# Optimization experiments

Hardware: AMD Instinct MI355X
Metric: run time of the kernel (lower is better)

The kernel has to match this reference:

```python
import jax, jax.numpy as jnp
import numpy as np

NHEADS = 8
LN_EPS = 1e-5

def _layer_norm(x, g, b):
    mu = jnp.mean(x, axis=-1, keepdims=True)
    var = jnp.mean((x - mu) ** 2, axis=-1, keepdims=True)
    return (x - mu) * jax.lax.rsqrt(var + LN_EPS) * g + b

def setup_inputs() -> dict:
    key = jax.random.key(0)
    ks = jax.random.split(key, 12)
    B, L, D = 8, 1024, 512
    F = 2 * D  # ffn_dim = 2*dim
    std = 0.01  # init_weights: Linear weights ~ N(0, 0.01), biases zero
    inp = {
        'query': jax.random.normal(ks[0], (B, L, D), dtype=jnp.float32),
        'q_mask': jnp.ones((B, L), dtype=jnp.int32),
        'wq': jax.random.normal(ks[1], (D, D), dtype=jnp.float32) * std,
        'bq': jnp.zeros((D,), dtype=jnp.float32),
        'wk': jax.random.normal(ks[2], (D, D), dtype=jnp.float32) * std,
        'bk': jnp.zeros((D,), dtype=jnp.float32),
        'wv': jax.random.normal(ks[3], (D, D), dtype=jnp.float32) * std,
        'bv': jnp.zeros((D,), dtype=jnp.float32),
        'wo': jax.random.normal(ks[4], (D, D), dtype=jnp.float32) * std,
        'bo': jnp.zeros((D,), dtype=jnp.float32),
        'ln1_g': jnp.ones((D,), dtype=jnp.float32),
        'ln1_b': jnp.zeros((D,), dtype=jnp.float32),
        'w1': jax.random.normal(ks[5], (D, F), dtype=jnp.float32) * std,
        'b1': jnp.zeros((F,), dtype=jnp.float32),
        'w2': jax.random.normal(ks[6], (F, D), dtype=jnp.float32) * std,
        'b2': jnp.zeros((D,), dtype=jnp.float32),
        'ln2_g': jnp.ones((D,), dtype=jnp.float32),
        'ln2_b': jnp.zeros((D,), dtype=jnp.float32),
    }
    return inp

def reference(query, q_mask, wq, bq, wk, bk, wv, bv, wo, bo, ln1_g, ln1_b, w1, b1, w2, b2, ln2_g, ln2_b):
    B, L, D = query.shape
    H = NHEADS
    dh = D // H
    residual = query
    # projections (dropout in eval mode -> identity)
    q = query @ wq + bq
    k = query @ wk + bk
    v = query @ wv + bv
    # faithful to torch .view(batch*nheads, -1, dim_head) (no head transpose)
    q = q.reshape(B * H, L, dh)
    k = k.reshape(B * H, L, dh)
    v = v.reshape(B * H, L, dh)
    # faithful to torch mask.repeat(nheads, 1) -> tile along batch dim
    mf = q_mask.astype(jnp.float32)
    qm = jnp.tile(mf, (H, 1))  # [B*H, L]
    km = qm
    mask = qm[:, :, None] * km[:, None, :]  # [B*H, L, L] outer product
    scores = jnp.einsum('bqd,bkd->bqk', q, k) / np.sqrt(dh).astype(np.float32)
    A = jnp.where(mask == 0, 0.0, jnp.exp(scores))  # masked_fill(-inf).exp()
    A_sum = jnp.maximum(jnp.sum(A, axis=-1, keepdims=True), 1.0)
    attn = A / A_sum
    context = jnp.einsum('bqk,bkd->bqd', attn, v).reshape(B, L, H * dh)
    out = context @ wo + bo
    out = _layer_norm(residual + out, ln1_g, ln1_b)
    # positional-wise FFN: Linear -> ReLU -> Linear, residual + LayerNorm
    ffn = jax.nn.relu(out @ w1 + b1) @ w2 + b2
    out2 = _layer_norm(out + ffn, ln2_g, ln2_b)
    return (out2, q_mask, query, query, q_mask)
```

## Files before the change

kernel.cpp:

```cpp
#include <hip/hip_runtime.h>
#include <hip/hip_bf16.h>

typedef __hip_bfloat16 bf16;
typedef __attribute__((ext_vector_type(4))) float f32x4;
typedef __attribute__((ext_vector_type(8))) short s16x8;

#define MFMA(a, b, c) __builtin_amdgcn_mfma_f32_16x16x32_bf16((a), (b), (c), 0, 0, 0)

__device__ __forceinline__ void g2l16(const bf16* g, bf16* l) {
  __builtin_amdgcn_global_load_lds((const __attribute__((address_space(1))) void*)g,
                                   (__attribute__((address_space(3))) void*)l,
                                   16, 0, 0);
}
__device__ __forceinline__ bf16 cvt_bf(float f) { return __float2bfloat16(f); }
__device__ __forceinline__ float bf2f(bf16 h) { return __bfloat162float(h); }

__global__ __launch_bounds__(256)
void wcvt_all_k(const float* __restrict__ wq, const float* __restrict__ wk,
                const float* __restrict__ wv, const float* __restrict__ wo,
                const float* __restrict__ w1, const float* __restrict__ w2,
                bf16* __restrict__ wqkvT, bf16* __restrict__ woT,
                bf16* __restrict__ w1T, bf16* __restrict__ w2T)
{
  __shared__ float tl[32][33];
  const int bid = blockIdx.x;
  const float* W; bf16* Wt; int K, N, tile;
  if (bid < 768)        { int s = bid >> 8; W = s==0?wq:(s==1?wk:wv);
                          Wt = wqkvT + s*262144; K = 512; N = 512; tile = bid & 255; }
  else if (bid < 1024)  { W = wo; Wt = woT; K = 512;  N = 512;  tile = bid - 768; }
  else if (bid < 1536)  { W = w1; Wt = w1T; K = 512;  N = 1024; tile = bid - 1024; }
  else                  { W = w2; Wt = w2T; K = 1024; N = 512;  tile = bid - 1536; }
  const int nx = N >> 5;
  const int n0 = (tile % nx) * 32, k0 = (tile / nx) * 32;
  const int tx = threadIdx.x & 31, ty = threadIdx.x >> 5;
#pragma unroll
  for (int i = 0; i < 32; i += 8)
    tl[ty + i][tx] = W[(size_t)(k0 + ty + i) * N + n0 + tx];
  __syncthreads();
#pragma unroll
  for (int i = 0; i < 32; i += 8)
    Wt[(size_t)(n0 + ty + i) * K + k0 + tx] = cvt_bf(tl[tx][ty + i]);
}

__global__ __launch_bounds__(256)
void cvt_k(const float* __restrict__ in, bf16* __restrict__ o)
{
  const int i = (blockIdx.x * 256 + threadIdx.x) * 8;
  float4 a = *(const float4*)(in + i);
  float4 b = *(const float4*)(in + i + 4);
  union { bf16 h[8]; s16x8 v; } u;
  u.h[0] = cvt_bf(a.x); u.h[1] = cvt_bf(a.y); u.h[2] = cvt_bf(a.z); u.h[3] = cvt_bf(a.w);
  u.h[4] = cvt_bf(b.x); u.h[5] = cvt_bf(b.y); u.h[6] = cvt_bf(b.z); u.h[7] = cvt_bf(b.w);
  *(s16x8*)(o + i) = u.v;
}

template<int BN, int EPI>
__global__ __launch_bounds__(256, 2)
void gemm_k(const bf16* __restrict__ A, const bf16* __restrict__ Bt,
            const float* __restrict__ b0, const float* __restrict__ b1,
            const float* __restrict__ b2,
            const float* __restrict__ rF, const bf16* __restrict__ rB,
            bf16* __restrict__ C0, bf16* __restrict__ C1, bf16* __restrict__ C2,
            int M, int Nout, int K)
{
  constexpr int NI = BN / 32;
  __shared__ bf16 As[128 * 64];
  __shared__ bf16 Bs[BN * 64];
  const int tid = threadIdx.x;
  const int wave = tid >> 6, lane = tid & 63;
  const int g = lane >> 4, c = lane & 15;
  const int m0 = blockIdx.x * 128, n0 = blockIdx.y * BN;
  const int wm = (wave >> 1) * 64, wn = (wave & 1) * (BN / 2);
  const int srl = lane >> 3;
  const int csub = ((lane & 7) ^ (lane >> 3)) * 8;

  f32x4 acc[4][NI];
#pragma unroll
  for (int i = 0; i < 4; ++i)
#pragma unroll
    for (int j = 0; j < NI; ++j) acc[i][j] = (f32x4)0.f;

  for (int k0 = 0; k0 < K; k0 += 64) {
#pragma unroll
    for (int is = 0; is < 4; ++is) {
      const int tr = wave * 32 + is * 8;
      g2l16(A + (size_t)(m0 + tr + srl) * K + (k0 + csub), As + tr * 64);
    }
#pragma unroll
    for (int is = 0; is < BN / 32; ++is) {
      const int tr = wave * (BN / 4) + is * 8;
      g2l16(Bt + (size_t)(n0 + tr + srl) * K + (k0 + csub), Bs + tr * 64);
    }
    __syncthreads();
#pragma unroll
    for (int ks = 0; ks < 2; ++ks) {
      s16x8 af[4], bfr[NI];
#pragma unroll
      for (int i = 0; i < 4; ++i) {
        const int ar = wm + i * 16 + c;
        af[i] = *(const s16x8*)((const char*)As + ar * 128 + ((ks * 4 + g) ^ (ar & 7)) * 16);
      }
#pragma unroll
      for (int i = 0; i < NI; ++i) {
        const int br = wn + i * 16 + c;
        bfr[i] = *(const s16x8*)((const char*)Bs + br * 128 + ((ks * 4 + g) ^ (br & 7)) * 16);
      }
#pragma unroll
      for (int mi = 0; mi < 4; ++mi)
#pragma unroll
        for (int ni = 0; ni < NI; ++ni)
          acc[mi][ni] = MFMA(af[mi], bfr[ni], acc[mi][ni]);
    }
    __syncthreads();
  }

  bf16* Cp; const float* bp; int colbase;
  if constexpr (EPI == 0) {
    const int seg = n0 >> 9;
    Cp = seg == 0 ? C0 : (seg == 1 ? C1 : C2);
    bp = seg == 0 ? b0 : (seg == 1 ? b1 : b2);
    colbase = n0 & 511;
  } else { Cp = C0; bp = b0; colbase = n0; }

#pragma unroll
  for (int ni = 0; ni < NI; ++ni) {
    const int col = colbase + wn + ni * 16 + c;
    const float bv = bp[col];
#pragma unroll
    for (int mi = 0; mi < 4; ++mi) {
#pragma unroll
      for (int r = 0; r < 4; ++r) {
        const int row = m0 + wm + mi * 16 + g * 4 + r;
        float v = acc[mi][ni][r] + bv;
        if constexpr (EPI == 1) v += rF[(size_t)row * Nout + col];
        if constexpr (EPI == 2) v = fmaxf(v, 0.f);
        if constexpr (EPI == 3) v += bf2f(rB[(size_t)row * Nout + col]);
        Cp[(size_t)row * Nout + col] = cvt_bf(v);
      }
    }
  }
}

__global__ __launch_bounds__(256)
void vtr_k(const bf16* __restrict__ V, bf16* __restrict__ Vt)
{
  __shared__ bf16 tl[64][72];
  const int bh = blockIdx.y, kt = blockIdx.x;
  const int r = threadIdx.x >> 2, c = threadIdx.x & 3;
  const bf16* src = V + (size_t)bh * 65536 + (size_t)(kt * 64 + r) * 64 + c * 16;
  *(s16x8*)&tl[r][c * 16]     = *(const s16x8*)(src);
  *(s16x8*)&tl[r][c * 16 + 8] = *(const s16x8*)(src + 8);
  __syncthreads();
  union { bf16 h[8]; s16x8 v; } u0, u1;
#pragma unroll
  for (int j = 0; j < 8; ++j) { u0.h[j] = tl[c * 16 + j][r]; u1.h[j] = tl[c * 16 + 8 + j][r]; }
  bf16* dst = Vt + (size_t)bh * 65536 + (size_t)r * 1024 + kt * 64 + c * 16;
  *(s16x8*)dst = u0.v;
  *(s16x8*)(dst + 8) = u1.v;
}

__global__ __launch_bounds__(256, 4)
void attn_k(const bf16* __restrict__ Q, const bf16* __restrict__ Kp,
            const bf16* __restrict__ Vt, const int* __restrict__ mask,
            bf16* __restrict__ ctx)
{
  __shared__ bf16 Ks[64 * 64];
  __shared__ bf16 Vs[64 * 64];
  __shared__ bf16 Ps[4][16 * 64];
  const int lane = threadIdx.x & 63, wave = threadIdx.x >> 6;
  const int g = lane >> 4, c = lane & 15;
  const int wg = blockIdx.x;
  const int swz = (wg & 7) * 128 + (wg >> 3);
  const int qb = swz & 15, bh = swz >> 4;
  const int q0 = qb * 64 + wave * 16;
  const bf16* Qg = Q  + (size_t)bh * 65536;
  const bf16* Kg = Kp + (size_t)bh * 65536;
  const bf16* Vg = Vt + (size_t)bh * 65536;
  const int* mrow = mask + (bh & 7) * 1024;
  bf16* Pw = Ps[wave];

  const s16x8 qa0 = *(const s16x8*)(Qg + (size_t)(q0 + c) * 64 + g * 8);
  const s16x8 qa1 = *(const s16x8*)(Qg + (size_t)(q0 + c) * 64 + 32 + g * 8);
  int mq[4];
#pragma unroll
  for (int r = 0; r < 4; ++r) mq[r] = mrow[q0 + g * 4 + r];

  s16x8 ones;
#pragma unroll
  for (int i = 0; i < 8; ++i) ones[i] = (short)0x3F80;

  f32x4 actx[4];
#pragma unroll
  for (int i = 0; i < 4; ++i) actx[i] = (f32x4)0.f;
  f32x4 asum = (f32x4)0.f;

  const int rl = lane >> 3, ch = lane & 7;
  const int schunk = (ch ^ rl) * 8;

  for (int kt = 0; kt < 16; ++kt) {
#pragma unroll
    for (int rnd = 0; rnd < 2; ++rnd) {
      const int rb = wave * 16 + rnd * 8;
      g2l16(Kg + (size_t)(kt * 64 + rb + rl) * 64 + schunk, Ks + rb * 64);
      g2l16(Vg + (size_t)(rb + rl) * 1024 + kt * 64 + schunk, Vs + rb * 64);
    }
    __syncthreads();

#pragma unroll
    for (int kb = 0; kb < 4; ++kb) {
      const int krow = kb * 16 + c;
      const char* kbase = (const char*)Ks + krow * 128;
      s16x8 kf0 = *(const s16x8*)(kbase + ((g    ) ^ (krow & 7)) * 16);
      s16x8 kf1 = *(const s16x8*)(kbase + ((g + 4) ^ (krow & 7)) * 16);
      f32x4 z = (f32x4)0.f;
      z = MFMA(qa0, kf0, z);
      z = MFMA(qa1, kf1, z);
      const int mk = mrow[kt * 64 + krow];
#pragma unroll
      for (int r = 0; r < 4; ++r) {
        const float e = (mk && mq[r]) ? __expf(z[r] * 0.125f) : 0.f;
        Pw[(g * 4 + r) * 64 + ((kb * 16 + c) ^ (g * 16))] = cvt_bf(e);
      }
    }

#pragma unroll
    for (int kk = 0; kk < 2; ++kk) {
      const s16x8 pa = *(const s16x8*)((const char*)Pw + c * 128
                         + 2 * ((kk * 32 + 8 * g) ^ ((c >> 2) << 4)));
      asum = MFMA(pa, ones, asum);
#pragma unroll
      for (int db = 0; db < 4; ++db) {
        const s16x8 vf = *(const s16x8*)((const char*)Vs + (db * 16 + c) * 128
                           + 16 * ((4 * kk + g) ^ (c & 7)));
        actx[db] = MFMA(pa, vf, actx[db]);
      }
    }
    __syncthreads();
  }

#pragma unroll
  for (int r = 0; r < 4; ++r) {
    const float inv = 1.f / fmaxf(asum[r], 1.f);
    const int qr = q0 + g * 4 + r;
#pragma unroll
    for (int db = 0; db < 4; ++db)
      ctx[(size_t)bh * 65536 + (size_t)qr * 64 + db * 16 + c] = cvt_bf(actx[db][r] * inv);
  }
}

template<int INB, int OUTF, int OUTB>
__global__ __launch_bounds__(256)
void ln_k(const void* __restrict__ xin, const float* __restrict__ g,
          const float* __restrict__ bb, float* __restrict__ of, bf16* __restrict__ ob)
{
  const int row = blockIdx.x * 4 + (threadIdx.x >> 6);
  const int lane = threadIdx.x & 63;
  float xv[8];
  if constexpr (INB) {
    union { s16x8 v; bf16 h[8]; } u;
    u.v = *(const s16x8*)((const bf16*)xin + (size_t)row * 512 + lane * 8);
#pragma unroll
    for (int j = 0; j < 8; ++j) xv[j] = bf2f(u.h[j]);
  } else {
    const float* xr = (const float*)xin + (size_t)row * 512 + lane * 8;
    float4 a = *(const float4*)xr, b = *(const float4*)(xr + 4);
    xv[0]=a.x; xv[1]=a.y; xv[2]=a.z; xv[3]=a.w; xv[4]=b.x; xv[5]=b.y; xv[6]=b.z; xv[7]=b.w;
  }
  float s = 0.f, q = 0.f;
#pragma unroll
  for (int j = 0; j < 8; ++j) { s += xv[j]; q += xv[j] * xv[j]; }
#pragma unroll
  for (int m = 1; m < 64; m <<= 1) { s += __shfl_xor(s, m); q += __shfl_xor(q, m); }
  const float mu = s * (1.f / 512.f);
  const float var = q * (1.f / 512.f) - mu * mu;
  const float rs = rsqrtf(var + 1e-5f);
  float4 g0 = *(const float4*)(g + lane * 8),  g1 = *(const float4*)(g + lane * 8 + 4);
  float4 b0 = *(const float4*)(bb + lane * 8), b1 = *(const float4*)(bb + lane * 8 + 4);
  float gv[8] = {g0.x, g0.y, g0.z, g0.w, g1.x, g1.y, g1.z, g1.w};
  float bv[8] = {b0.x, b0.y, b0.z, b0.w, b1.x, b1.y, b1.z, b1.w};
  float ov[8];
#pragma unroll
  for (int j = 0; j < 8; ++j) ov[j] = (xv[j] - mu) * rs * gv[j] + bv[j];
  if constexpr (OUTF) {
    float4 o0 = {ov[0], ov[1], ov[2], ov[3]};
    float4 o1 = {ov[4], ov[5], ov[6], ov[7]};
    float* outr = of + (size_t)row * 512 + lane * 8;
    *(float4*)outr = o0;
    *(float4*)(outr + 4) = o1;
  }
  if constexpr (OUTB) {
    union { bf16 h[8]; s16x8 v; } u;
#pragma unroll
    for (int j = 0; j < 8; ++j) u.h[j] = cvt_bf(ov[j]);
    *(s16x8*)(ob + (size_t)row * 512 + lane * 8) = u.v;
  }
}

__global__ __launch_bounds__(256)
void mask_k(const int* __restrict__ m, float* __restrict__ out)
{
  const int i = blockIdx.x * 256 + threadIdx.x;
  const float v = (float)m[i];
  out[4194304 + i] = v;
  out[12591104 + i] = v;
}

extern "C" void kernel_launch(void* const* d_in, const int* in_sizes, int n_in,
                              void* d_out, int out_size, void* d_ws, size_t ws_size,
                              hipStream_t stream)
{
  const float* query = (const float*)d_in[0];
  const int*   qmask = (const int*)d_in[1];
  const float* wq = (const float*)d_in[2];
  const float* bq = (const float*)d_in[3];
  const float* wk = (const float*)d_in[4];
  const float* bk = (const float*)d_in[5];
  const float* wv = (const float*)d_in[6];
  const float* bv = (const float*)d_in[7];
  const float* wo = (const float*)d_in[8];
  const float* bo = (const float*)d_in[9];
  const float* ln1g = (const float*)d_in[10];
  const float* ln1b = (const float*)d_in[11];
  const float* w1 = (const float*)d_in[12];
  const float* b1 = (const float*)d_in[13];
  const float* w2 = (const float*)d_in[14];
  const float* b2 = (const float*)d_in[15];
  const float* ln2g = (const float*)d_in[16];
  const float* ln2b = (const float*)d_in[17];
  float* out = (float*)d_out;
  char* ws = (char*)d_ws;
  char* ob = (char*)d_out;

  bf16* wqkvT = (bf16*)(ws);
  bf16* woT   = (bf16*)(ws + 1572864);
  bf16* w1T   = (bf16*)(ws + 2097152);
  bf16* w2T   = (bf16*)(ws + 3145728);

  char* R0 = ob;
  char* R1 = ob + 16809984;
  char* R2 = ob + 33587200;
  bf16*  qb    = (bf16*)R0;
  bf16*  ctx   = (bf16*)R0;
  bf16*  x1b   = (bf16*)R0;
  bf16*  Qb    = (bf16*)R1;
  bf16*  Kb    = (bf16*)(R1 + 8388608);
  bf16*  attnr = (bf16*)R1;
  bf16*  hbuf  = (bf16*)R1;
  bf16*  Vb    = (bf16*)R2;
  bf16*  VtG   = (bf16*)(R2 + 8388608);
  bf16*  ybuf  = (bf16*)R2;

  const dim3 blk(256);

  wcvt_all_k<<<2048, blk, 0, stream>>>(wq, wk, wv, wo, w1, w2, wqkvT, woT, w1T, w2T);
  cvt_k<<<2048, blk, 0, stream>>>(query, qb);

  gemm_k<128, 0><<<dim3(64, 12), blk, 0, stream>>>(qb, wqkvT, bq, bk, bv,
      nullptr, nullptr, Qb, Kb, Vb, 8192, 512, 512);

  vtr_k<<<dim3(16, 64), blk, 0, stream>>>(Vb, VtG);

  attn_k<<<1024, blk, 0, stream>>>(Qb, Kb, VtG, qmask, ctx);

  gemm_k<64, 1><<<dim3(64, 8), blk, 0, stream>>>(ctx, woT, bo, nullptr, nullptr,
      query, nullptr, attnr, nullptr, nullptr, 8192, 512, 512);

  ln_k<1, 0, 1><<<2048, blk, 0, stream>>>(attnr, ln1g, ln1b, nullptr, x1b);

  gemm_k<128, 2><<<dim3(64, 8), blk, 0, stream>>>(x1b, w1T, b1, nullptr, nullptr,
      nullptr, nullptr, hbuf, nullptr, nullptr, 8192, 1024, 512);

  gemm_k<64, 3><<<dim3(64, 8), blk, 0, stream>>>(hbuf, w2T, b2, nullptr, nullptr,
      nullptr, x1b, ybuf, nullptr, nullptr, 8192, 512, 1024);

  ln_k<1, 1, 0><<<2048, blk, 0, stream>>>(ybuf, ln2g, ln2b, out, nullptr);

  mask_k<<<32, blk, 0, stream>>>(qmask, out);
  hipMemcpyAsync(out + 4202496, query, 16777216, hipMemcpyDeviceToDevice, stream);
  hipMemcpyAsync(out + 8396800, query, 16777216, hipMemcpyDeviceToDevice, stream);
}
```

Before: 246.3 us.

## Double-buffer K/V tiles, keep P in registers, and process two query strips per wave

Restructures the attention kernel. K/V tiles are now double-buffered in LDS so the next tile's global-to-LDS loads overlap compute. Scores are computed with swapped MFMA operands so the exp'd probabilities land directly in the register layout the PV MFMA needs, which removes the LDS round-trip for P. Each wave now handles 32 query rows, reusing the K/V fragments across them, with half as many blocks. The key mask becomes an additive -1e30 offset precomputed in LDS and the query mask is applied at the end. The cost is higher register pressure (occupancy hint lowered to 2), fewer blocks, and a permuted K row staging order that has to match the transposed output layout.

Result: faster. 225.6 us (-8.4%).

```diff
diff --git a/kernel.cpp b/kernel.cpp
--- a/kernel.cpp
+++ b/kernel.cpp
@@ -159,93 +159,135 @@
   *(s16x8*)(dst + 8) = u1.v;
 }
 
-__global__ __launch_bounds__(256, 4)
+__global__ __launch_bounds__(256, 2)
 void attn_k(const bf16* __restrict__ Q, const bf16* __restrict__ Kp,
             const bf16* __restrict__ Vt, const int* __restrict__ mask,
             bf16* __restrict__ ctx)
 {
-  __shared__ bf16 Ks[64 * 64];
-  __shared__ bf16 Vs[64 * 64];
-  __shared__ bf16 Ps[4][16 * 64];
+  __shared__ bf16 Ks[2][64 * 64];
+  __shared__ bf16 Vs[2][64 * 64];
+  __shared__ __align__(16) float koff[1024];
   const int lane = threadIdx.x & 63, wave = threadIdx.x >> 6;
   const int g = lane >> 4, c = lane & 15;
   const int wg = blockIdx.x;
-  const int swz = (wg & 7) * 128 + (wg >> 3);
-  const int qb = swz & 15, bh = swz >> 4;
-  const int q0 = qb * 64 + wave * 16;
+  const int swz = (wg & 7) * 64 + (wg >> 3);
+  const int qb = swz & 7, bh = swz >> 3;
+  const int q0w = qb * 128 + wave * 32;
   const bf16* Qg = Q  + (size_t)bh * 65536;
   const bf16* Kg = Kp + (size_t)bh * 65536;
   const bf16* Vg = Vt + (size_t)bh * 65536;
   const int* mrow = mask + (bh & 7) * 1024;
-  bf16* Pw = Ps[wave];
-
-  const s16x8 qa0 = *(const s16x8*)(Qg + (size_t)(q0 + c) * 64 + g * 8);
-  const s16x8 qa1 = *(const s16x8*)(Qg + (size_t)(q0 + c) * 64 + 32 + g * 8);
-  int mq[4];
-#pragma unroll
-  for (int r = 0; r < 4; ++r) mq[r] = mrow[q0 + g * 4 + r];
+
+  {
+    const int i = threadIdx.x * 4;
+    int4 m4 = *(const int4*)(mrow + i);
+    f32x4 kv;
+    kv[0] = m4.x ? 0.f : -1e30f;
+    kv[1] = m4.y ? 0.f : -1e30f;
+    kv[2] = m4.z ? 0.f : -1e30f;
+    kv[3] = m4.w ? 0.f : -1e30f;
+    *(f32x4*)&koff[i] = kv;
+  }
+
+  s16x8 qa[2][2];
+#pragma unroll
+  for (int qs = 0; qs < 2; ++qs)
+#pragma unroll
+    for (int h = 0; h < 2; ++h)
+      qa[qs][h] = *(const s16x8*)(Qg + (size_t)(q0w + qs * 16 + c) * 64 + h * 32 + g * 8);
+
+  float qm[2][4];
+#pragma unroll
+  for (int qs = 0; qs < 2; ++qs)
+#pragma unroll
+    for (int r = 0; r < 4; ++r)
+      qm[qs][r] = mrow[q0w + qs * 16 + g * 4 + r] ? 1.f : 0.f;
 
   s16x8 ones;
 #pragma unroll
   for (int i = 0; i < 8; ++i) ones[i] = (short)0x3F80;
 
-  f32x4 actx[4];
-#pragma unroll
-  for (int i = 0; i < 4; ++i) actx[i] = (f32x4)0.f;
-  f32x4 asum = (f32x4)0.f;
+  f32x4 acc[2][4], asum[2];
+#pragma unroll
+  for (int qs = 0; qs < 2; ++qs) {
+    asum[qs] = (f32x4)0.f;
+#pragma unroll
+    for (int db = 0; db < 4; ++db) acc[qs][db] = (f32x4)0.f;
+  }
 
   const int rl = lane >> 3, ch = lane & 7;
   const int schunk = (ch ^ rl) * 8;
 
-  for (int kt = 0; kt < 16; ++kt) {
+  auto STAGE = [&](int kt, int buf) {
 #pragma unroll
     for (int rnd = 0; rnd < 2; ++rnd) {
       const int rb = wave * 16 + rnd * 8;
-      g2l16(Kg + (size_t)(kt * 64 + rb + rl) * 64 + schunk, Ks + rb * 64);
-      g2l16(Vg + (size_t)(rb + rl) * 1024 + kt * 64 + schunk, Vs + rb * 64);
-    }
-    __syncthreads();
+      const int l = rb + rl;
+      const int i16 = l & 15, kbb = l >> 4;
+      const int srow = ((kbb >> 1) << 5) + ((i16 >> 2) << 3) + ((kbb & 1) << 2) + (i16 & 3);
+      g2l16(Kg + (size_t)(kt * 64 + srow) * 64 + schunk, &Ks[buf][rb * 64]);
+      g2l16(Vg + (size_t)l * 1024 + kt * 64 + schunk, &Vs[buf][rb * 64]);
+    }
+  };
+
+  STAGE(0, 0);
+  __syncthreads();
+
+  for (int kt = 0; kt < 16; ++kt) {
+    const int cur = kt & 1;
+    if (kt < 15) STAGE(kt + 1, cur ^ 1);
+
+    union { unsigned w[8]; s16x8 v[2]; } pr[2];
 
 #pragma unroll
     for (int kb = 0; kb < 4; ++kb) {
       const int krow = kb * 16 + c;
-      const char* kbase = (const char*)Ks + krow * 128;
-      s16x8 kf0 = *(const s16x8*)(kbase + ((g    ) ^ (krow & 7)) * 16);
-      s16x8 kf1 = *(const s16x8*)(kbase + ((g + 4) ^ (krow & 7)) * 16);
-      f32x4 z = (f32x4)0.f;
-      z = MFMA(qa0, kf0, z);
-      z = MFMA(qa1, kf1, z);
-      const int mk = mrow[kt * 64 + krow];
-#pragma unroll
-      for (int r = 0; r < 4; ++r) {
-        const float e = (mk && mq[r]) ? __expf(z[r] * 0.125f) : 0.f;
-        Pw[(g * 4 + r) * 64 + ((kb * 16 + c) ^ (g * 16))] = cvt_bf(e);
+      const char* kbase = (const char*)&Ks[cur][0] + krow * 128;
+      const s16x8 kf0 = *(const s16x8*)(kbase + ((g    ) ^ (c & 7)) * 16);
+      const s16x8 kf1 = *(const s16x8*)(kbase + ((g + 4) ^ (c & 7)) * 16);
+      const f32x4 ko = *(const f32x4*)&koff[kt * 64 + ((kb >> 1) << 5) + (g << 3) + ((kb & 1) << 2)];
+#pragma unroll
+      for (int qs = 0; qs < 2; ++qs) {
+        f32x4 z = (f32x4)0.f;
+        z = MFMA(kf0, qa[qs][0], z);
+        z = MFMA(kf1, qa[qs][1], z);
+        union { bf16 h[4]; unsigned u[2]; } eh;
+#pragma unroll
+        for (int r = 0; r < 4; ++r)
+          eh.h[r] = cvt_bf(__expf(fmaf(z[r], 0.125f, ko[r])));
+        pr[qs].w[kb * 2]     = eh.u[0];
+        pr[qs].w[kb * 2 + 1] = eh.u[1];
       }
     }
 
 #pragma unroll
     for (int kk = 0; kk < 2; ++kk) {
-      const s16x8 pa = *(const s16x8*)((const char*)Pw + c * 128
-                         + 2 * ((kk * 32 + 8 * g) ^ ((c >> 2) << 4)));
-      asum = MFMA(pa, ones, asum);
-#pragma unroll
-      for (int db = 0; db < 4; ++db) {
-        const s16x8 vf = *(const s16x8*)((const char*)Vs + (db * 16 + c) * 128
-                           + 16 * ((4 * kk + g) ^ (c & 7)));
-        actx[db] = MFMA(pa, vf, actx[db]);
+      s16x8 vf[4];
+#pragma unroll
+      for (int db = 0; db < 4; ++db)
+        vf[db] = *(const s16x8*)((const char*)&Vs[cur][0] + (db * 16 + c) * 128 + ((4 * kk + g) ^ (c & 7)) * 16);
+#pragma unroll
+      for (int qs = 0; qs < 2; ++qs) {
+        const s16x8 pa = pr[qs].v[kk];
+        asum[qs] = MFMA(pa, ones, asum[qs]);
+#pragma unroll
+        for (int db = 0; db < 4; ++db)
+          acc[qs][db] = MFMA(pa, vf[db], acc[qs][db]);
       }
     }
     __syncthreads();
   }
 
 #pragma unroll
-  for (int r = 0; r < 4; ++r) {
-    const float inv = 1.f / fmaxf(asum[r], 1.f);
-    const int qr = q0 + g * 4 + r;
-#pragma unroll
-    for (int db = 0; db < 4; ++db)
-      ctx[(size_t)bh * 65536 + (size_t)qr * 64 + db * 16 + c] = cvt_bf(actx[db][r] * inv);
-  }
+  for (int qs = 0; qs < 2; ++qs)
+#pragma unroll
+    for (int r = 0; r < 4; ++r) {
+      const float inv = qm[qs][r] / fmaxf(asum[qs][r], 1.f);
+      const size_t qr = q0w + qs * 16 + g * 4 + r;
+#pragma unroll
+      for (int db = 0; db < 4; ++db)
+        ctx[(size_t)bh * 65536 + qr * 64 + db * 16 + c] = cvt_bf(acc[qs][db][r] * inv);
+    }
 }
 
 template<int INB, int OUTF, int OUTB>
@@ -360,7 +402,7 @@
 
   vtr_k<<<dim3(16, 64), blk, 0, stream>>>(Vb, VtG);
 
-  attn_k<<<1024, blk, 0, stream>>>(Qb, Kb, VtG, qmask, ctx);
+  attn_k<<<512, blk, 0, stream>>>(Qb, Kb, VtG, qmask, ctx);
 
   gemm_k<64, 1><<<dim3(64, 8), blk, 0, stream>>>(ctx, woT, bo, nullptr, nullptr,
       query, nullptr, attnr, nullptr, nullptr, 8192, 512, 512);
```
